# Kernel optimization log

Hardware: AMD Instinct MI355X
Metric: run time of the kernel (lower is better)

The kernel has to match this reference:

```python
import jax, jax.numpy as jnp
import numpy as np

CHANNELS = [(3, 64), (64, 64), (64, 128), (128, 128), (128, 256), (256, 256), (256, 256),
            (256, 512), (512, 512), (512, 512), (512, 512), (512, 512), (512, 512)]
HW = 256
IN_FEAT = 512 * (HW // 32) * (HW // 32)  # 32768


def _conv(x, w):
    # 3x3, stride 1, pad 1, NCHW / OIHW, no bias
    return jax.lax.conv_general_dilated(x, w, (1, 1), ((1, 1), (1, 1)),
                                         dimension_numbers=("NCHW", "OIHW", "NCHW"))


def _maxpool2(x):
    return jax.lax.reduce_window(x, -jnp.inf, jax.lax.max, (1, 1, 2, 2), (1, 1, 2, 2), "VALID")


def setup_inputs() -> dict:
    key = jax.random.key(0)
    keys = jax.random.split(key, 17)
    inp = {"x": jax.random.normal(keys[0], (1, 3, HW, HW), jnp.float32),
           "H": HW, "W": HW, "nTh": 32, "nTw": 32}
    for i, (cin, cout) in enumerate(CHANNELS):
        scale = (1.0 / np.sqrt(9.0 * cin)).astype(np.float32) if hasattr(np.sqrt(9.0 * cin), 'astype') else 1.0 / np.sqrt(9.0 * cin)
        inp[f"cw{i + 1}"] = jax.random.normal(keys[1 + i], (cout, cin, 3, 3), jnp.float32) * np.float32(1.0 / np.sqrt(9.0 * cin))
    inp["fw1"] = jax.random.normal(keys[14], (4096, IN_FEAT), jnp.float32) * np.float32(1.0 / np.sqrt(IN_FEAT))
    inp["fw2"] = jax.random.normal(keys[15], (4096, 4096), jnp.float32) * np.float32(1.0 / np.sqrt(4096))
    inp["fw3"] = jax.random.normal(keys[16], (1000, 4096), jnp.float32) * np.float32(1.0 / np.sqrt(4096))
    return inp


def reference(x, H, W, nTh, nTw, cw1, cw2, cw3, cw4, cw5, cw6, cw7, cw8, cw9, cw10,
              cw11, cw12, cw13, fw1, fw2, fw3):
    # VGG-16 conv stack; tiling in the original is an execution schedule only,
    # the math equals the untiled stack. conv -> relu repeated, maxpool per block.
    conv_ws = [cw1, cw2, cw3, cw4, cw5, cw6, cw7, cw8, cw9, cw10, cw11, cw12, cw13]
    blocks = [(0, 2), (2, 4), (4, 7), (7, 10), (10, 13)]
    h = x
    for lo, hi in blocks:
        for w in conv_ws[lo:hi]:
            h = jax.nn.relu(_conv(h, w))
        h = _maxpool2(h)
    h = h.reshape(h.shape[0], -1)          # [1, 32768]
    h = h @ fw1.T                           # fc1 (no bias, no relu, as in source)
    h = h @ fw2.T                           # fc2
    h = h @ fw3.T                           # fc3 -> [1, 1000]
    return h
```

## Files before the change

### kernel.cpp

```cpp
#include <hip/hip_runtime.h>
#include <cstddef>


typedef __attribute__((ext_vector_type(8))) short short8;
typedef __attribute__((ext_vector_type(4))) float f32x4;

__device__ inline unsigned short f2bf(float f) {
    unsigned int u = __builtin_bit_cast(unsigned int, f);
    u += 0x7FFF + ((u >> 16) & 1);
    return (unsigned short)(u >> 16);
}

__device__ __forceinline__ void gl_lds16(const void* src, unsigned m0v) {
    asm volatile("s_mov_b32 m0, %1\n\t"
                 "global_load_lds_dwordx4 %0, off"
                 :: "v"(src), "s"(m0v) : "memory");
}

struct WtDesc { const float* src; unsigned dst; int cin; int cout; int blk0; };
struct WtArgs { WtDesc d[12]; };

__global__ __launch_bounds__(256)
void wt_all_k(WtArgs A, unsigned short* __restrict__ wt, unsigned short* __restrict__ guard)
{
    __shared__ unsigned short lds[4][9 * 520];
    const int tid = threadIdx.x, wv = tid >> 6, lane = tid & 63;
    if (blockIdx.x == 0 && tid < 128) guard[tid] = 0;

    int l = 0;
#pragma unroll
    for (int i = 1; i < 12; ++i) l = ((int)blockIdx.x >= A.d[i].blk0) ? i : l;
    const WtDesc D = A.d[l];
    const int co = ((int)blockIdx.x - D.blk0) * 4 + wv;
    const int n = D.cin * 9;
    const int cinP = D.cin + 8;

    const float4* src = (const float4*)(D.src + (size_t)co * n);
    for (int i = lane; i < (n >> 2); i += 64) {
        float4 v = src[i];
        unsigned short b[4] = {f2bf(v.x), f2bf(v.y), f2bf(v.z), f2bf(v.w)};
        const int f0 = i * 4;
#pragma unroll
        for (int k = 0; k < 4; ++k) {
            const int f = f0 + k, ci = f / 9, pos = f - ci * 9;
            lds[wv][pos * cinP + ci] = b[k];
        }
    }
    __syncthreads();
    unsigned short* dstb = wt + D.dst;
#pragma unroll 1
    for (int pos = 0; pos < 9; ++pos) {
        unsigned short* drow = dstb + ((size_t)pos * D.cout + co) * D.cin;
        for (int c4 = lane; c4 < (D.cin >> 2); c4 += 64) {
            ushort4 u = *(const ushort4*)&lds[wv][pos * cinP + c4 * 4];
            *(ushort4*)(drow + c4 * 4) = u;
        }
    }
}

template<int PR, int CO, int MODE>
__global__ __launch_bounds__(256, 2)
void conv_mfma_k(const unsigned short* __restrict__ act,
                 const unsigned short* __restrict__ wt,
                 const unsigned short* __restrict__ guard,
                 void* __restrict__ outp,
                 int Cin, int Cout, int H, int W)
{
    constexpr int NT = (PR + 3) / 4;
    constexpr int MT = CO / 16;
    constexpr int ICELLS = (PR + 2) * 18;
    constexpr int ITASK = ICELLS * 4;
    constexpr int ITIN = (ITASK + 255) / 256;
    constexpr int IBYTES = ((ITASK + 63) & ~63) * 16;
    constexpr int WTASK = 9 * CO * 4;
    constexpr int WIT = (WTASK + 255) / 256;
    constexpr int WBYTES = 9 * CO * 64;
    constexpr int VL = WIT + ITIN;
    static_assert(VL == 7 || VL == 8 || VL == 11, "unexpected stage depth");
    static_assert(MODE == 0 || ((MODE == 3 || MODE == 4) && (NT % 2) == 0), "pool needs even NT");

    __shared__ __align__(16) unsigned short wLds[2 * WBYTES / 2];
    __shared__ __align__(16) unsigned short iLds[2 * IBYTES / 2];
    __shared__ __align__(16) unsigned short dump[512];

    const int tid = threadIdx.x;
    const int lane = tid & 63, wv = tid >> 6;
    const int half = lane >> 4, l15 = lane & 15;
    const int tilesX = W >> 4;
    const int pY = blockIdx.x / tilesX, pX = blockIdx.x - pY * tilesX;
    const int y0 = pY * PR, x0 = pX * 16;
    const int cob = blockIdx.y;
    const int nCh = Cin >> 5;

    f32x4 acc[MT][NT];
#pragma unroll
    for (int mt = 0; mt < MT; ++mt)
#pragma unroll
        for (int nt = 0; nt < NT; ++nt) acc[mt][nt] = (f32x4){0.f, 0.f, 0.f, 0.f};

    auto STAGE = [&](int buf, int ci0) {
        const unsigned wB = (unsigned)(size_t)wLds + buf * WBYTES;
        const unsigned iB = (unsigned)(size_t)iLds + buf * IBYTES;
        const unsigned dB = (unsigned)(size_t)dump;
#pragma unroll
        for (int it = 0; it < WIT; ++it) {
            const int idx = it * 256 + tid;
            const int cell = idx >> 2, q = idx & 3;
            const int pos = cell / CO, co = cell % CO;
            const bool real = idx < WTASK;
            const unsigned short* src = real ?
                wt + (size_t)(pos * Cout + cob * CO + co) * Cin + ci0 + q * 8 : guard;
            const bool eng = (it * 256 + wv * 64) < WTASK;
            gl_lds16(src, __builtin_amdgcn_readfirstlane(
                eng ? wB + (unsigned)(it * 4096 + wv * 1024) : dB));
        }
#pragma unroll
        for (int it = 0; it < ITIN; ++it) {
            const int idx = it * 256 + tid;
            const int cell = idx >> 2, q = idx & 3;
            const int r = cell / 18, c = cell - r * 18;
            const int y = y0 - 1 + r, x = x0 - 1 + c;
            const bool ok = (idx < ITASK) & (y >= 0) & (y < H) & (x >= 0) & (x < W);
            const unsigned short* src = ok ?
                act + (size_t)(y * W + x) * Cin + ci0 + q * 8 : guard;
            const bool eng = (it * 256 + wv * 64) < ITASK;
            gl_lds16(src, __builtin_amdgcn_readfirstlane(
                eng ? iB + (unsigned)(it * 4096 + wv * 1024) : dB));
        }
    };

    STAGE(0, 0);
    for (int t = 0; t < nCh; ++t) {
        const int buf = t & 1;
        if (t + 1 < nCh) {
            STAGE(buf ^ 1, (t + 1) << 5);
            if constexpr (VL == 7)  asm volatile("s_waitcnt vmcnt(7)" ::: "memory");
            else if constexpr (VL == 8)  asm volatile("s_waitcnt vmcnt(8)" ::: "memory");
            else asm volatile("s_waitcnt vmcnt(11)" ::: "memory");
        } else {
            asm volatile("s_waitcnt vmcnt(0)" ::: "memory");
        }
        __builtin_amdgcn_s_barrier();
        asm volatile("" ::: "memory");

        const unsigned short* wP = wLds + buf * (WBYTES / 2);
        const unsigned short* iP = iLds + buf * (IBYTES / 2);
#pragma unroll
        for (int ky = 0; ky < 3; ++ky)
#pragma unroll
        for (int kx = 0; kx < 3; ++kx) {
            const int pos = ky * 3 + kx;
            short8 a[MT];
#pragma unroll
            for (int mt = 0; mt < MT; ++mt)
                a[mt] = *(const short8*)&wP[((pos * CO) + (mt << 4) + l15) * 32 + half * 8];
#pragma unroll
            for (int nt = 0; nt < NT; ++nt) {
                const short8 b = *(const short8*)
                    &iP[((wv * NT + nt + ky) * 18 + l15 + kx) * 32 + half * 8];
#pragma unroll
                for (int mt = 0; mt < MT; ++mt)
                    acc[mt][nt] = __builtin_amdgcn_mfma_f32_16x16x32_bf16(a[mt], b, acc[mt][nt], 0, 0, 0);
            }
        }
        asm volatile("" ::: "memory");
        __builtin_amdgcn_s_barrier();
    }

    const int xg = x0 + l15;
    if constexpr (MODE == 3 || MODE == 4) {
        const int Wo = W >> 1;
#pragma unroll
        for (int mt = 0; mt < MT; ++mt)
#pragma unroll
        for (int nt = 0; nt < NT; nt += 2) {
            f32x4 a;
#pragma unroll
            for (int j = 0; j < 4; ++j) a[j] = fmaxf(acc[mt][nt][j], acc[mt][nt + 1][j]);
            f32x4 m;
#pragma unroll
            for (int j = 0; j < 4; ++j) m[j] = fmaxf(a[j], __shfl_xor(a[j], 1, 64));
            if ((l15 & 1) == 0) {
                const int yo = (y0 + wv * NT + nt) >> 1;
                const int xo = xg >> 1;
                const int co = cob * CO + (mt << 4) + half * 4;
                if constexpr (MODE == 3) {
                    ushort4 u;
                    u.x = f2bf(fmaxf(m[0], 0.f));
                    u.y = f2bf(fmaxf(m[1], 0.f));
                    u.z = f2bf(fmaxf(m[2], 0.f));
                    u.w = f2bf(fmaxf(m[3], 0.f));
                    *(ushort4*)((unsigned short*)outp + ((size_t)(yo * Wo + xo) * Cout + co)) = u;
                } else {
                    const int Ho = W >> 1;  (void)Ho;
                    float* op = (float*)outp;
                    const int hw = (W >> 1) * (W >> 1);
#pragma unroll
                    for (int j = 0; j < 4; ++j)
                        op[(size_t)(co + j) * hw + yo * Wo + xo] = fmaxf(m[j], 0.f);
                }
            }
        }
    } else {
#pragma unroll
        for (int mt = 0; mt < MT; ++mt)
#pragma unroll
        for (int nt = 0; nt < NT; ++nt) {
            const int yg = y0 + wv * NT + nt;
            const int co = cob * CO + (mt << 4) + half * 4;
            const size_t base = (size_t)(yg * W + xg) * Cout + co;
            ushort4 u;
            u.x = f2bf(fmaxf(acc[mt][nt][0], 0.f));
            u.y = f2bf(fmaxf(acc[mt][nt][1], 0.f));
            u.z = f2bf(fmaxf(acc[mt][nt][2], 0.f));
            u.w = f2bf(fmaxf(acc[mt][nt][3], 0.f));
            *(ushort4*)((unsigned short*)outp + base) = u;
        }
    }
}

#define TILE 16
#define COB  32
__global__ __launch_bounds__(256)
void conv1_k(const float* __restrict__ in, const float* __restrict__ wt,
             unsigned short* __restrict__ out)
{
    const int Cin = 3, H = 256, W = 256, HW = H * W;
    __shared__ float sIn[2][648];
    __shared__ float sWt[2][768];

    const int tid = threadIdx.x;
    const int bx = blockIdx.x, by = blockIdx.y, co_blk = blockIdx.z;
    const int co_grp = tid >> 6;
    const int lane = tid & 63;
    const int tx = lane & 7, ty = lane >> 3;
    const int x0 = bx * TILE, y0 = by * TILE;

    int iLdsI[3], iG[3], iSub[3]; bool iOk[3];
    int wLdsI[3], wG[3], wSub[3]; bool wOk[3];
#pragma unroll
    for (int j = 0; j < 3; ++j) {
        int i = tid + j * 256;
        iOk[j] = false; iLdsI[j] = 0; iG[j] = 0; iSub[j] = 0;
        if (i < 648) {
            int sub = i / 324; int r = i - sub * 324;
            int iy = r / 18;   int ix = r - iy * 18;
            iSub[j] = sub; iLdsI[j] = sub * 324 + r;
            int y = y0 - 1 + iy, x = x0 - 1 + ix;
            if (y >= 0 && y < H && x >= 0 && x < W) { iOk[j] = true; iG[j] = sub * HW + y * W + x; }
        }
        wOk[j] = false; wLdsI[j] = 0; wG[j] = 0; wSub[j] = 0;
        if (i < 576) {
            int sub = i / 288; int r = i - sub * 288;
            int col = r / 9;   int k = r - col * 9;
            wSub[j] = sub; wLdsI[j] = sub * 384 + col * 12 + k;
            wG[j] = ((co_blk * COB + col) * Cin + sub) * 9 + k;
            wOk[j] = true;
        }
    }

    float4 acc[8];
#pragma unroll
    for (int c = 0; c < 8; ++c) acc[c] = make_float4(0.f, 0.f, 0.f, 0.f);

    const int nSteps = 2;
    float rIn[3], rWt[3];
    {
#pragma unroll
        for (int j = 0; j < 3; ++j)
            rIn[j] = (iOk[j] && iSub[j] < 3) ? in[iG[j]] : 0.f;
#pragma unroll
        for (int j = 0; j < 3; ++j)
            rWt[j] = (wOk[j] && wSub[j] < 3) ? wt[wG[j]] : 0.f;
#pragma unroll
        for (int j = 0; j < 3; ++j) { if (tid + j * 256 < 648) sIn[0][iLdsI[j]] = rIn[j]; }
#pragma unroll
        for (int j = 0; j < 3; ++j) { if (tid + j * 256 < 576) sWt[0][wLdsI[j]] = rWt[j]; }
    }

    for (int t = 0; t < nSteps; ++t) {
        __syncthreads();
        const bool more = (t + 1) < nSteps;
        if (more) {
            const int ci0 = 2;
#pragma unroll
            for (int j = 0; j < 3; ++j)
                rIn[j] = (iOk[j] && (ci0 + iSub[j]) < 3) ? in[(size_t)ci0 * HW + iG[j]] : 0.f;
#pragma unroll
            for (int j = 0; j < 3; ++j)
                rWt[j] = (wOk[j] && (ci0 + wSub[j]) < 3) ? wt[(size_t)ci0 * 9 + wG[j]] : 0.f;
        }
        const int buf = t & 1;
        const float* sI = sIn[buf];
        const float* sW = sWt[buf];
#pragma unroll
        for (int sub = 0; sub < 2; ++sub) {
            float wv[4][4];
            const float* sp = sI + sub * 324 + (2 * ty) * 18 + 2 * tx;
#pragma unroll
            for (int r = 0; r < 4; ++r) {
                float2 a = *(const float2*)(sp + r * 18);
                float2 b = *(const float2*)(sp + r * 18 + 2);
                wv[r][0] = a.x; wv[r][1] = a.y; wv[r][2] = b.x; wv[r][3] = b.y;
            }
#pragma unroll
            for (int c = 0; c < 8; ++c) {
                const float* wp = sW + sub * 384 + (co_grp * 8 + c) * 12;
                float4 w0 = *(const float4*)wp;
                float4 w1 = *(const float4*)(wp + 4);
                float  w8 = wp[8];
                const float wk[9] = {w0.x, w0.y, w0.z, w0.w, w1.x, w1.y, w1.z, w1.w, w8};
                float* ac = (float*)&acc[c];
#pragma unroll
                for (int py = 0; py < 2; ++py)
#pragma unroll
                for (int px = 0; px < 2; ++px) {
                    float sacc = ac[py * 2 + px];
#pragma unroll
                    for (int kk = 0; kk < 9; ++kk)
                        sacc = fmaf(wv[py + kk / 3][px + kk % 3], wk[kk], sacc);
                    ac[py * 2 + px] = sacc;
                }
            }
        }
        if (more) {
#pragma unroll
            for (int j = 0; j < 3; ++j) { if (tid + j * 256 < 648) sIn[buf ^ 1][iLdsI[j]] = rIn[j]; }
#pragma unroll
            for (int j = 0; j < 3; ++j) { if (tid + j * 256 < 576) sWt[buf ^ 1][wLdsI[j]] = rWt[j]; }
        }
    }

    const int co0 = co_blk * COB + co_grp * 8;
#pragma unroll
    for (int py = 0; py < 2; ++py)
#pragma unroll
    for (int px = 0; px < 2; ++px) {
        const int y = y0 + 2 * ty + py, x = x0 + 2 * tx + px;
        unsigned short u8[8];
#pragma unroll
        for (int c = 0; c < 8; ++c)
            u8[c] = f2bf(fmaxf(((const float*)&acc[c])[py * 2 + px], 0.f));
        *(uint4*)(out + (size_t)(y * W + x) * 64 + co0) = *(uint4*)u8;
    }
}

__global__ __launch_bounds__(256)
void gemv_k(const float* __restrict__ Wm, const float* __restrict__ xv,
            float* __restrict__ y, int K)
{
    __shared__ float red[4];
    const int tid = threadIdx.x;
    const float4* row = (const float4*)(Wm + (size_t)blockIdx.x * K);
    const float4* x4  = (const float4*)xv;
    const int K4 = K >> 2;
    float sum = 0.f;
    for (int i = tid; i < K4; i += 256) {
        float4 a = row[i], b = x4[i];
        sum += a.x * b.x + a.y * b.y + a.z * b.z + a.w * b.w;
    }
#pragma unroll
    for (int off = 32; off > 0; off >>= 1) sum += __shfl_down(sum, off, 64);
    if ((tid & 63) == 0) red[tid >> 6] = sum;
    __syncthreads();
    if (tid == 0) y[blockIdx.x] = red[0] + red[1] + red[2] + red[3];
}

extern "C" void kernel_launch(void* const* d_in, const int* in_sizes, int n_in,
                              void* d_out, int out_size, void* d_ws, size_t ws_size,
                              hipStream_t stream)
{
    (void)in_sizes; (void)n_in; (void)out_size; (void)ws_size;
    const float* x = (const float*)d_in[0];
    const float* cw[13];
    for (int i = 0; i < 13; ++i) cw[i] = (const float*)d_in[5 + i];
    const float* fw1 = (const float*)d_in[18];
    const float* fw2 = (const float*)d_in[19];
    const float* fw3 = (const float*)d_in[20];
    float* outp = (float*)d_out;

    static const int CIN[12]  = {64, 64, 128, 128, 256, 256, 256, 512, 512, 512, 512, 512};
    static const int COUT[12] = {64, 128, 128, 256, 256, 256, 512, 512, 512, 512, 512, 512};

    char* ws = (char*)d_ws;
    size_t wOff[12]; size_t o = 0;
    for (int i = 0; i < 12; ++i) { wOff[i] = o; o += (size_t)9 * COUT[i] * CIN[i]; }
    unsigned short* WT = (unsigned short*)ws;
    unsigned short* guardp = WT + o;
    size_t ao = ((o + 128) * 2 + 255) & ~(size_t)255;
    unsigned short* bA = (unsigned short*)(ws + ao);
    unsigned short* bB = (unsigned short*)(ws + ao + 8388608);
    float* fcIn = (float*)bA;
    float* F1 = (float*)bB;
    float* F2 = F1 + 4096;

    WtArgs wa; int blk = 0;
    {
        size_t oo = 0;
        for (int i = 0; i < 12; ++i) {
            wa.d[i].src = cw[i + 1];
            wa.d[i].dst = (unsigned)oo;
            wa.d[i].cin = CIN[i];
            wa.d[i].cout = COUT[i];
            wa.d[i].blk0 = blk;
            oo += (size_t)9 * COUT[i] * CIN[i];
            blk += COUT[i] / 4;
        }
    }
    wt_all_k<<<blk, 256, 0, stream>>>(wa, WT, guardp);

    conv1_k<<<dim3(16, 16, 2), 256, 0, stream>>>(x, cw[0], bA);

    conv_mfma_k<16, 32, 3><<<dim3(256, 2), 256, 0, stream>>>(bA, WT + wOff[0], guardp, bB, 64, 64, 256, 256);
    conv_mfma_k<8, 32, 0><<<dim3(128, 4), 256, 0, stream>>>(bB, WT + wOff[1], guardp, bA, 64, 128, 128, 128);
    conv_mfma_k<8, 32, 3><<<dim3(128, 4), 256, 0, stream>>>(bA, WT + wOff[2], guardp, bB, 128, 128, 128, 128);
    conv_mfma_k<8, 32, 0><<<dim3(32, 8), 256, 0, stream>>>(bB, WT + wOff[3], guardp, bA, 128, 256, 64, 64);
    conv_mfma_k<8, 32, 0><<<dim3(32, 8), 256, 0, stream>>>(bA, WT + wOff[4], guardp, bB, 256, 256, 64, 64);
    conv_mfma_k<8, 32, 3><<<dim3(32, 8), 256, 0, stream>>>(bB, WT + wOff[5], guardp, bA, 256, 256, 64, 64);
    conv_mfma_k<4, 32, 0><<<dim3(16, 16), 256, 0, stream>>>(bA, WT + wOff[6], guardp, bB, 256, 512, 32, 32);
    conv_mfma_k<4, 32, 0><<<dim3(16, 16), 256, 0, stream>>>(bB, WT + wOff[7], guardp, bA, 512, 512, 32, 32);
    conv_mfma_k<8, 32, 3><<<dim3(8, 16), 256, 0, stream>>>(bA, WT + wOff[8], guardp, bB, 512, 512, 32, 32);
    conv_mfma_k<4, 32, 0><<<dim3(4, 16), 256, 0, stream>>>(bB, WT + wOff[9], guardp, bA, 512, 512, 16, 16);
    conv_mfma_k<4, 32, 0><<<dim3(4, 16), 256, 0, stream>>>(bA, WT + wOff[10], guardp, bB, 512, 512, 16, 16);
    conv_mfma_k<8, 32, 4><<<dim3(2, 16), 256, 0, stream>>>(bB, WT + wOff[11], guardp, fcIn, 512, 512, 16, 16);

    gemv_k<<<4096, 256, 0, stream>>>(fw1, fcIn, F1, 32768);
    gemv_k<<<4096, 256, 0, stream>>>(fw2, F1, F2, 4096);
    gemv_k<<<1000, 256, 0, stream>>>(fw3, F2, outp, 4096);
}
```

Baseline: 940.5 us.

## Fuse weight prep and conv stack into one persistent kernel with grid barriers

Merges the weight-transpose kernel, first conv and all twelve MFMA conv layers into a single 512-block persistent kernel. Layers are separated by a software grid barrier built on an atomic counter that is reset with a memset. This removes per-layer launch overhead and the drain/fill gaps between kernels. In exchange, late layers leave most blocks idle, every block waits at a barrier, and correctness relies on all 512 blocks being co-resident (256 CUs times 2 blocks each with about 80 KB of LDS).

Result: slower. 1.454 ms (+54.7%).

```diff
diff --git a/kernel.cpp b/kernel.cpp
--- a/kernel.cpp
+++ b/kernel.cpp
@@ -17,21 +17,29 @@
                  :: "v"(src), "s"(m0v) : "memory");
 }
 
+__device__ __forceinline__ void gridbar(unsigned* cnt, unsigned& gen, unsigned nblk)
+{
+    __syncthreads();
+    if (threadIdx.x == 0) {
+        gen += nblk;
+        __threadfence();
+        __hip_atomic_fetch_add(cnt, 1u, __ATOMIC_RELAXED, __HIP_MEMORY_SCOPE_AGENT);
+        while (__hip_atomic_load(cnt, __ATOMIC_RELAXED, __HIP_MEMORY_SCOPE_AGENT) < gen)
+            __builtin_amdgcn_s_sleep(8);
+        __threadfence();
+    }
+    __syncthreads();
+}
+
 struct WtDesc { const float* src; unsigned dst; int cin; int cout; int blk0; };
 struct WtArgs { WtDesc d[12]; };
 
-__global__ __launch_bounds__(256)
-void wt_all_k(WtArgs A, unsigned short* __restrict__ wt, unsigned short* __restrict__ guard)
-{
-    __shared__ unsigned short lds[4][9 * 520];
-    const int tid = threadIdx.x, wv = tid >> 6, lane = tid & 63;
-    if (blockIdx.x == 0 && tid < 128) guard[tid] = 0;
-
-    int l = 0;
-#pragma unroll
-    for (int i = 1; i < 12; ++i) l = ((int)blockIdx.x >= A.d[i].blk0) ? i : l;
-    const WtDesc D = A.d[l];
-    const int co = ((int)blockIdx.x - D.blk0) * 4 + wv;
+__device__ void wt_body(const WtDesc& D, int relvb, unsigned short* __restrict__ wt,
+                        char* smem, int tid)
+{
+    unsigned short* lds = (unsigned short*)smem + (tid >> 6) * 4680;
+    const int wv = tid >> 6, lane = tid & 63;
+    const int co = relvb * 4 + wv;
     const int n = D.cin * 9;
     const int cinP = D.cin + 8;
 
@@ -43,7 +51,7 @@
 #pragma unroll
         for (int k = 0; k < 4; ++k) {
             const int f = f0 + k, ci = f / 9, pos = f - ci * 9;
-            lds[wv][pos * cinP + ci] = b[k];
+            lds[pos * cinP + ci] = b[k];
         }
     }
     __syncthreads();
@@ -52,19 +60,20 @@
     for (int pos = 0; pos < 9; ++pos) {
         unsigned short* drow = dstb + ((size_t)pos * D.cout + co) * D.cin;
         for (int c4 = lane; c4 < (D.cin >> 2); c4 += 64) {
-            ushort4 u = *(const ushort4*)&lds[wv][pos * cinP + c4 * 4];
+            ushort4 u = *(const ushort4*)&lds[pos * cinP + c4 * 4];
             *(ushort4*)(drow + c4 * 4) = u;
         }
     }
+    (void)wv;
 }
 
 template<int PR, int CO, int MODE>
-__global__ __launch_bounds__(256, 2)
-void conv_mfma_k(const unsigned short* __restrict__ act,
+__device__ void conv_body(char* smem,
+                 const unsigned short* __restrict__ act,
                  const unsigned short* __restrict__ wt,
                  const unsigned short* __restrict__ guard,
                  void* __restrict__ outp,
-                 int Cin, int Cout, int H, int W)
+                 int Cin, int Cout, int H, int W, int vx, int vy, int tid)
 {
     constexpr int NT = (PR + 3) / 4;
     constexpr int MT = CO / 16;
@@ -79,17 +88,16 @@
     static_assert(VL == 7 || VL == 8 || VL == 11, "unexpected stage depth");
     static_assert(MODE == 0 || ((MODE == 3 || MODE == 4) && (NT % 2) == 0), "pool needs even NT");
 
-    __shared__ __align__(16) unsigned short wLds[2 * WBYTES / 2];
-    __shared__ __align__(16) unsigned short iLds[2 * IBYTES / 2];
-    __shared__ __align__(16) unsigned short dump[512];
-
-    const int tid = threadIdx.x;
+    unsigned short* wLds = (unsigned short*)smem;
+    unsigned short* iLds = (unsigned short*)(smem + 36864);
+    unsigned short* dump = (unsigned short*)(smem + 79872);
+
     const int lane = tid & 63, wv = tid >> 6;
     const int half = lane >> 4, l15 = lane & 15;
     const int tilesX = W >> 4;
-    const int pY = blockIdx.x / tilesX, pX = blockIdx.x - pY * tilesX;
+    const int pY = vx / tilesX, pX = vx - pY * tilesX;
     const int y0 = pY * PR, x0 = pX * 16;
-    const int cob = blockIdx.y;
+    const int cob = vy;
     const int nCh = Cin >> 5;
 
     f32x4 acc[MT][NT];
@@ -192,7 +200,6 @@
                     u.w = f2bf(fmaxf(m[3], 0.f));
                     *(ushort4*)((unsigned short*)outp + ((size_t)(yo * Wo + xo) * Cout + co)) = u;
                 } else {
-                    const int Ho = W >> 1;  (void)Ho;
                     float* op = (float*)outp;
                     const int hw = (W >> 1) * (W >> 1);
 #pragma unroll
@@ -221,16 +228,14 @@
 
 #define TILE 16
 #define COB  32
-__global__ __launch_bounds__(256)
-void conv1_k(const float* __restrict__ in, const float* __restrict__ wt,
-             unsigned short* __restrict__ out)
+__device__ void conv1_body(const float* __restrict__ in, const float* __restrict__ wt,
+                           unsigned short* __restrict__ out, char* smem, int vb, int tid)
 {
     const int Cin = 3, H = 256, W = 256, HW = H * W;
-    __shared__ float sIn[2][648];
-    __shared__ float sWt[2][768];
-
-    const int tid = threadIdx.x;
-    const int bx = blockIdx.x, by = blockIdx.y, co_blk = blockIdx.z;
+    float* sIn = (float*)smem;
+    float* sWt = (float*)(smem + 5184);
+
+    const int bx = vb & 15, by = (vb >> 4) & 15, co_blk = vb >> 8;
     const int co_grp = tid >> 6;
     const int lane = tid & 63;
     const int tx = lane & 7, ty = lane >> 3;
@@ -273,9 +278,9 @@
         for (int j = 0; j < 3; ++j)
             rWt[j] = (wOk[j] && wSub[j] < 3) ? wt[wG[j]] : 0.f;
 #pragma unroll
-        for (int j = 0; j < 3; ++j) { if (tid + j * 256 < 648) sIn[0][iLdsI[j]] = rIn[j]; }
-#pragma unroll
-        for (int j = 0; j < 3; ++j) { if (tid + j * 256 < 576) sWt[0][wLdsI[j]] = rWt[j]; }
+        for (int j = 0; j < 3; ++j) { if (tid + j * 256 < 648) sIn[iLdsI[j]] = rIn[j]; }
+#pragma unroll
+        for (int j = 0; j < 3; ++j) { if (tid + j * 256 < 576) sWt[wLdsI[j]] = rWt[j]; }
     }
 
     for (int t = 0; t < nSteps; ++t) {
@@ -291,8 +296,8 @@
                 rWt[j] = (wOk[j] && (ci0 + wSub[j]) < 3) ? wt[(size_t)ci0 * 9 + wG[j]] : 0.f;
         }
         const int buf = t & 1;
-        const float* sI = sIn[buf];
-        const float* sW = sWt[buf];
+        const float* sI = sIn + buf * 648;
+        const float* sW = sWt + buf * 768;
 #pragma unroll
         for (int sub = 0; sub < 2; ++sub) {
             float wv[4][4];
@@ -324,10 +329,11 @@
             }
         }
         if (more) {
-#pragma unroll
-            for (int j = 0; j < 3; ++j) { if (tid + j * 256 < 648) sIn[buf ^ 1][iLdsI[j]] = rIn[j]; }
-#pragma unroll
-            for (int j = 0; j < 3; ++j) { if (tid + j * 256 < 576) sWt[buf ^ 1][wLdsI[j]] = rWt[j]; }
+            const int b2 = buf ^ 1;
+#pragma unroll
+            for (int j = 0; j < 3; ++j) { if (tid + j * 256 < 648) sIn[b2 * 648 + iLdsI[j]] = rIn[j]; }
+#pragma unroll
+            for (int j = 0; j < 3; ++j) { if (tid + j * 256 < 576) sWt[b2 * 768 + wLdsI[j]] = rWt[j]; }
         }
     }
 
@@ -343,6 +349,61 @@
             u8[c] = f2bf(fmaxf(((const float*)&acc[c])[py * 2 + px], 0.f));
         *(uint4*)(out + (size_t)(y * W + x) * 64 + co0) = *(uint4*)u8;
     }
+}
+
+struct UberArgs {
+    const float* x; const float* cw0;
+    WtArgs wt;
+    unsigned short* WT;
+    unsigned short* guard;
+    unsigned short* bA;
+    unsigned short* bB;
+    float* fcIn;
+    unsigned* cnt;
+    unsigned wOff[12];
+};
+
+__global__ __launch_bounds__(256, 2)
+void uber_k(UberArgs A)
+{
+    __shared__ __align__(16) char smem[80896];
+    const int bid = blockIdx.x, tid = threadIdx.x;
+    unsigned gen = 0;
+
+    if (bid == 0 && tid < 128) A.guard[tid] = 0;
+    conv1_body(A.x, A.cw0, A.bA, smem, bid, tid);
+    __syncthreads();
+    for (int vb = bid; vb < 1040; vb += 512) {
+        int l = 0;
+#pragma unroll
+        for (int i = 1; i < 12; ++i) l = (vb >= A.wt.d[i].blk0) ? i : l;
+        wt_body(A.wt.d[l], vb - A.wt.d[l].blk0, A.WT, smem, tid);
+        __syncthreads();
+    }
+    gridbar(A.cnt, gen, 512);
+    conv_body<16, 32, 3>(smem, A.bA, A.WT + A.wOff[0], A.guard, A.bB, 64, 64, 256, 256, bid & 255, bid >> 8, tid);
+    gridbar(A.cnt, gen, 512);
+    conv_body<8, 32, 0>(smem, A.bB, A.WT + A.wOff[1], A.guard, A.bA, 64, 128, 128, 128, bid & 127, bid >> 7, tid);
+    gridbar(A.cnt, gen, 512);
+    conv_body<8, 32, 3>(smem, A.bA, A.WT + A.wOff[2], A.guard, A.bB, 128, 128, 128, 128, bid & 127, bid >> 7, tid);
+    gridbar(A.cnt, gen, 512);
+    if (bid < 256) conv_body<8, 32, 0>(smem, A.bB, A.WT + A.wOff[3], A.guard, A.bA, 128, 256, 64, 64, bid & 31, bid >> 5, tid);
+    gridbar(A.cnt, gen, 512);
+    if (bid < 256) conv_body<8, 32, 0>(smem, A.bA, A.WT + A.wOff[4], A.guard, A.bB, 256, 256, 64, 64, bid & 31, bid >> 5, tid);
+    gridbar(A.cnt, gen, 512);
+    if (bid < 256) conv_body<8, 32, 3>(smem, A.bB, A.WT + A.wOff[5], A.guard, A.bA, 256, 256, 64, 64, bid & 31, bid >> 5, tid);
+    gridbar(A.cnt, gen, 512);
+    if (bid < 256) conv_body<4, 32, 0>(smem, A.bA, A.WT + A.wOff[6], A.guard, A.bB, 256, 512, 32, 32, bid & 15, bid >> 4, tid);
+    gridbar(A.cnt, gen, 512);
+    if (bid < 256) conv_body<4, 32, 0>(smem, A.bB, A.WT + A.wOff[7], A.guard, A.bA, 512, 512, 32, 32, bid & 15, bid >> 4, tid);
+    gridbar(A.cnt, gen, 512);
+    if (bid < 128) conv_body<8, 32, 3>(smem, A.bA, A.WT + A.wOff[8], A.guard, A.bB, 512, 512, 32, 32, bid & 7, bid >> 3, tid);
+    gridbar(A.cnt, gen, 512);
+    if (bid < 64) conv_body<4, 32, 0>(smem, A.bB, A.WT + A.wOff[9], A.guard, A.bA, 512, 512, 16, 16, bid & 3, bid >> 2, tid);
+    gridbar(A.cnt, gen, 512);
+    if (bid < 64) conv_body<4, 32, 0>(smem, A.bA, A.WT + A.wOff[10], A.guard, A.bB, 512, 512, 16, 16, bid & 3, bid >> 2, tid);
+    gridbar(A.cnt, gen, 512);
+    if (bid < 32) conv_body<8, 32, 4>(smem, A.bB, A.WT + A.wOff[11], A.guard, A.fcIn, 512, 512, 16, 16, bid & 1, bid >> 1, tid);
 }
 
 __global__ __launch_bounds__(256)
@@ -390,39 +451,32 @@
     size_t ao = ((o + 128) * 2 + 255) & ~(size_t)255;
     unsigned short* bA = (unsigned short*)(ws + ao);
     unsigned short* bB = (unsigned short*)(ws + ao + 8388608);
+    unsigned* cnt = (unsigned*)(ws + ao + 2 * 8388608);
     float* fcIn = (float*)bA;
     float* F1 = (float*)bB;
     float* F2 = F1 + 4096;
 
-    WtArgs wa; int blk = 0;
+    hipMemsetAsync(cnt, 0, 256, stream);
+
+    UberArgs ua;
+    ua.x = x; ua.cw0 = cw[0];
     {
-        size_t oo = 0;
+        int blk = 0; size_t oo = 0;
         for (int i = 0; i < 12; ++i) {
-            wa.d[i].src = cw[i + 1];
-            wa.d[i].dst = (unsigned)oo;
-            wa.d[i].cin = CIN[i];
-            wa.d[i].cout = COUT[i];
-            wa.d[i].blk0 = blk;
+            ua.wt.d[i].src = cw[i + 1];
+            ua.wt.d[i].dst = (unsigned)oo;
+            ua.wt.d[i].cin = CIN[i];
+            ua.wt.d[i].cout = COUT[i];
+            ua.wt.d[i].blk0 = blk;
             oo += (size_t)9 * COUT[i] * CIN[i];
             blk += COUT[i] / 4;
         }
     }
-    wt_all_k<<<blk, 256, 0, stream>>>(wa, WT, guardp);
-
-    conv1_k<<<dim3(16, 16, 2), 256, 0, stream>>>(x, cw[0], bA);
-
-    conv_mfma_k<16, 32, 3><<<dim3(256, 2), 256, 0, stream>>>(bA, WT + wOff[0], guardp, bB, 64, 64, 256, 256);
-    conv_mfma_k<8, 32, 0><<<dim3(128, 4), 256, 0, stream>>>(bB, WT + wOff[1], guardp, bA, 64, 128, 128, 128);
-    conv_mfma_k<8, 32, 3><<<dim3(128, 4), 256, 0, stream>>>(bA, WT + wOff[2], guardp, bB, 128, 128, 128, 128);
-    conv_mfma_k<8, 32, 0><<<dim3(32, 8), 256, 0, stream>>>(bB, WT + wOff[3], guardp, bA, 128, 256, 64, 64);
-    conv_mfma_k<8, 32, 0><<<dim3(32, 8), 256, 0, stream>>>(bA, WT + wOff[4], guardp, bB, 256, 256, 64, 64);
-    conv_mfma_k<8, 32, 3><<<dim3(32, 8), 256, 0, stream>>>(bB, WT + wOff[5], guardp, bA, 256, 256, 64, 64);
-    conv_mfma_k<4, 32, 0><<<dim3(16, 16), 256, 0, stream>>>(bA, WT + wOff[6], guardp, bB, 256, 512, 32, 32);
-    conv_mfma_k<4, 32, 0><<<dim3(16, 16), 256, 0, stream>>>(bB, WT + wOff[7], guardp, bA, 512, 512, 32, 32);
-    conv_mfma_k<8, 32, 3><<<dim3(8, 16), 256, 0, stream>>>(bA, WT + wOff[8], guardp, bB, 512, 512, 32, 32);
-    conv_mfma_k<4, 32, 0><<<dim3(4, 16), 256, 0, stream>>>(bB, WT + wOff[9], guardp, bA, 512, 512, 16, 16);
-    conv_mfma_k<4, 32, 0><<<dim3(4, 16), 256, 0, stream>>>(bA, WT + wOff[10], guardp, bB, 512, 512, 16, 16);
-    conv_mfma_k<8, 32, 4><<<dim3(2, 16), 256, 0, stream>>>(bB, WT + wOff[11], guardp, fcIn, 512, 512, 16, 16);
+    ua.WT = WT; ua.guard = guardp; ua.bA = bA; ua.bB = bB;
+    ua.fcIn = fcIn; ua.cnt = cnt;
+    for (int i = 0; i < 12; ++i) ua.wOff[i] = (unsigned)wOff[i];
+
+    uber_k<<<512, 256, 0, stream>>>(ua);
 
     gemv_k<<<4096, 256, 0, stream>>>(fw1, fcIn, F1, 32768);
     gemv_k<<<4096, 256, 0, stream>>>(fw2, F1, F2, 4096);
```
